# Optimization experiments

Measured on AMD Instinct MI355X. Metric: run time of the kernel, lower is better.

Reference implementation:

```python
import jax, jax.numpy as jnp
import numpy as np

B, IN, OUT = 512, 4096, 11008


def setup_inputs() -> dict:
    key = jax.random.key(0)
    k_x, k_stored, k_sign, k_scale, k_bias = jax.random.split(key, 5)
    x = jax.random.normal(k_x, (B, IN), dtype=jnp.float32)
    # QINS encoding: stored uint8 magnitude in [1, 255], sign in {-1, +1}
    stored = jax.random.randint(k_stored, (OUT, IN), 1, 256, dtype=jnp.int32)
    sign = 2 * jax.random.randint(k_sign, (OUT, IN), 0, 2, dtype=jnp.int32) - 1
    # log-range from from_linear's fallback calibration: weights in [e^-10, e^0]
    log_min = jnp.asarray(-10.0, dtype=jnp.float32)
    log_max = jnp.asarray(0.0, dtype=jnp.float32)
    # per-channel calibration scale, clamped to [0.5, 2.0] in from_linear
    scale = jax.random.uniform(k_scale, (OUT,), dtype=jnp.float32, minval=0.5, maxval=2.0)
    bias = jax.random.normal(k_bias, (OUT,), dtype=jnp.float32) * 0.01
    return {"x": x, "stored": stored, "sign": sign, "log_min": log_min,
            "log_max": log_max, "scale": scale, "bias": bias}


def reference(x, stored, sign, log_min, log_max, scale, bias):
    # Reconstruct fp32 weight from log-scale uint8 encoding (QINS)
    normalized = (255.0 - stored.astype(jnp.float32)) / 254.0      # [OUT, IN]
    log_w = log_min + normalized * (log_max - log_min)
    weight = sign.astype(jnp.float32) * jnp.exp(log_w)             # [OUT, IN]
    # y = (x @ W^T + b) * scale   (per-output-channel scale)
    out = jnp.einsum('bi,oi->bo', x, weight) + bias
    return out * scale
```

## Files before the change

kernel.cpp:

```cpp
#include <hip/hip_runtime.h>
#include <hip/hip_bf16.h>

#define B_DIM   512
#define IN_DIM  4096
#define OUT_DIM 11008

typedef __bf16 bf16x4 __attribute__((ext_vector_type(4)));
typedef __bf16 bf16x8 __attribute__((ext_vector_type(8)));
typedef float  floatx4 __attribute__((ext_vector_type(4)));

__global__ __launch_bounds__(256) void conv_x_kernel(
    const float* __restrict__ x, __bf16* __restrict__ xb) {
  int idx = blockIdx.x * blockDim.x + threadIdx.x;
  float4 v = ((const float4*)x)[idx];
  bf16x4 o;
  o[0] = (__bf16)v.x; o[1] = (__bf16)v.y; o[2] = (__bf16)v.z; o[3] = (__bf16)v.w;
  ((bf16x4*)xb)[idx] = o;
}

__device__ __forceinline__ void gl_lds16(const __bf16* g, __bf16* l) {
  __builtin_amdgcn_global_load_lds(
      (const __attribute__((address_space(1))) void*)g,
      (__attribute__((address_space(3))) void*)l, 16, 0, 0);
}

__device__ __forceinline__ void memfence_barrier() {
  asm volatile("" ::: "memory");
  __builtin_amdgcn_s_barrier();
  asm volatile("" ::: "memory");
}

__device__ __forceinline__ __bf16 dec1(int s, int g, float lmin, float slope) {
  return (__bf16)(__expf(lmin + (float)(255 - s) * slope) * (float)g);
}

__global__ __launch_bounds__(256, 2) void fused_qins_gemm_kernel(
    const __bf16* __restrict__ A,
    const int* __restrict__ stored,
    const int* __restrict__ sign,
    const float* __restrict__ logmin, const float* __restrict__ logmax,
    const float* __restrict__ scale, const float* __restrict__ bias,
    float* __restrict__ out) {
  constexpr int K = IN_DIM, N = OUT_DIM;
  constexpr int BK = 32;

  __shared__ __align__(16) __bf16 sA[2 * 128 * BK];
  __shared__ __align__(16) __bf16 sB[128 * BK];

  const int tid  = threadIdx.x;
  const int lane = tid & 63;
  const int wave = tid >> 6;
  const int wm   = (wave >> 1) * 64;
  const int wn   = (wave & 1) * 64;
  const int m16  = lane & 15;
  const int q    = lane >> 4;

  const int wg  = blockIdx.x;
  const int g   = (wg & 7) * 43 + (wg >> 3);
  const int bn0 = (g >> 2) * 128;
  const int bm0 = (g & 3) * 128;

  const float lmin  = logmin[0];
  const float slope = (logmax[0] - lmin) * (1.0f / 254.0f);

  const int r0 = tid >> 2;
  const int c0 = (tid & 3) * 8;
  const __bf16* gA0 = A + (bm0 + r0) * K + c0;
  const __bf16* gA1 = A + (bm0 + r0 + 64) * K + c0;

  const int rB = tid >> 1;
  const int kh = (tid & 1) * 16;
  const int* pS = stored + (size_t)(bn0 + rB) * K + kh;
  const int* pG = sign   + (size_t)(bn0 + rB) * K + kh;
  __bf16* lB = sB + rB * BK + kh;

  floatx4 acc[4][4] = {};

  gl_lds16(gA0, sA + tid * 8);
  gl_lds16(gA1, sA + 2048 + tid * 8);
  int4 s0 = ((const int4*)pS)[0], s1 = ((const int4*)pS)[1],
       s2 = ((const int4*)pS)[2], s3 = ((const int4*)pS)[3];
  int4 g0 = ((const int4*)pG)[0], g1 = ((const int4*)pG)[1],
       g2 = ((const int4*)pG)[2], g3 = ((const int4*)pG)[3];

  for (int kt = 0; kt < K; kt += BK) {
    const int cur = (kt >> 5) & 1;
    __bf16* sAc = sA + cur * 4096;
    __bf16* sAn = sA + (cur ^ 1) * 4096;

    bf16x8 w0, w1;
    w0[0] = dec1(s0.x, g0.x, lmin, slope);
    w0[1] = dec1(s0.y, g0.y, lmin, slope);
    w0[2] = dec1(s0.z, g0.z, lmin, slope);
    w0[3] = dec1(s0.w, g0.w, lmin, slope);
    w0[4] = dec1(s1.x, g1.x, lmin, slope);
    w0[5] = dec1(s1.y, g1.y, lmin, slope);
    w0[6] = dec1(s1.z, g1.z, lmin, slope);
    w0[7] = dec1(s1.w, g1.w, lmin, slope);
    w1[0] = dec1(s2.x, g2.x, lmin, slope);
    w1[1] = dec1(s2.y, g2.y, lmin, slope);
    w1[2] = dec1(s2.z, g2.z, lmin, slope);
    w1[3] = dec1(s2.w, g2.w, lmin, slope);
    w1[4] = dec1(s3.x, g3.x, lmin, slope);
    w1[5] = dec1(s3.y, g3.y, lmin, slope);
    w1[6] = dec1(s3.z, g3.z, lmin, slope);
    w1[7] = dec1(s3.w, g3.w, lmin, slope);

    memfence_barrier();

    *(bf16x8*)lB       = w0;
    *(bf16x8*)(lB + 8) = w1;

    asm volatile("s_waitcnt vmcnt(0) lgkmcnt(0)" ::: "memory");

    if (kt + BK < K) {
      gl_lds16(gA0 + kt + BK, sAn + tid * 8);
      gl_lds16(gA1 + kt + BK, sAn + 2048 + tid * 8);
      const int4* nS = (const int4*)(pS + kt + BK);
      const int4* nG = (const int4*)(pG + kt + BK);
      s0 = nS[0]; s1 = nS[1]; s2 = nS[2]; s3 = nS[3];
      g0 = nG[0]; g1 = nG[1]; g2 = nG[2]; g3 = nG[3];
    }

    memfence_barrier();

    bf16x8 afr[4], bfr[4];
#pragma unroll
    for (int i = 0; i < 4; ++i)
      afr[i] = *(const bf16x8*)&sAc[(wm + i * 16 + m16) * BK + q * 8];
#pragma unroll
    for (int i = 0; i < 4; ++i)
      bfr[i] = *(const bf16x8*)&sB[(wn + i * 16 + m16) * BK + q * 8];

#pragma unroll
    for (int mi = 0; mi < 4; ++mi)
#pragma unroll
      for (int ni = 0; ni < 4; ++ni)
        acc[mi][ni] = __builtin_amdgcn_mfma_f32_16x16x32_bf16(
            afr[mi], bfr[ni], acc[mi][ni], 0, 0, 0);
  }

#pragma unroll
  for (int ni = 0; ni < 4; ++ni) {
    const int col = bn0 + wn + ni * 16 + m16;
    const float sc = scale[col];
    const float bb = bias[col] * sc;
#pragma unroll
    for (int mi = 0; mi < 4; ++mi) {
#pragma unroll
      for (int r = 0; r < 4; ++r) {
        const int row = bm0 + wm + mi * 16 + q * 4 + r;
        out[row * N + col] = acc[mi][ni][r] * sc + bb;
      }
    }
  }
}

extern "C" void kernel_launch(void* const* d_in, const int* in_sizes, int n_in,
                              void* d_out, int out_size, void* d_ws, size_t ws_size,
                              hipStream_t stream) {
  const float* x      = (const float*)d_in[0];
  const int*   stored = (const int*)d_in[1];
  const int*   sign   = (const int*)d_in[2];
  const float* logmin = (const float*)d_in[3];
  const float* logmax = (const float*)d_in[4];
  const float* scale  = (const float*)d_in[5];
  const float* bias   = (const float*)d_in[6];
  float* out = (float*)d_out;

  __bf16* wsX = (__bf16*)d_ws;

  conv_x_kernel<<<2048, 256, 0, stream>>>(x, wsX);
  fused_qins_gemm_kernel<<<344, 256, 0, stream>>>(
      wsX, stored, sign, logmin, logmax, scale, bias, out);
}
```

Before: 516.8 us.

## Halve N tile, prefetch weights two stages ahead, and swizzle/pad LDS

The output tile shrinks from 128x128 to 128x64, doubling the grid to 688 workgroups so more CUs stay busy, and each thread decodes 8 weights per step instead of 16. The stored/sign int loads are now issued two K-steps ahead through a manually unrolled double-register pipeline, with a partial vmcnt wait instead of a full drain. The A tile uses an XOR swizzle and the B tile a padded row stride to reduce LDS bank conflicts. In exchange, each block reuses A over fewer columns, so total A traffic roughly doubles, and the final prefetches wrap around to redundant loads at k=0.

```diff
diff --git a/kernel.cpp b/kernel.cpp
--- a/kernel.cpp
+++ b/kernel.cpp
@@ -34,6 +34,20 @@
   return (__bf16)(__expf(lmin + (float)(255 - s) * slope) * (float)g);
 }
 
+__device__ __forceinline__ bf16x8 dec8(int4 sl, int4 sh, int4 gl, int4 gh,
+                                       float lmin, float slope) {
+  bf16x8 w;
+  w[0] = dec1(sl.x, gl.x, lmin, slope);
+  w[1] = dec1(sl.y, gl.y, lmin, slope);
+  w[2] = dec1(sl.z, gl.z, lmin, slope);
+  w[3] = dec1(sl.w, gl.w, lmin, slope);
+  w[4] = dec1(sh.x, gh.x, lmin, slope);
+  w[5] = dec1(sh.y, gh.y, lmin, slope);
+  w[6] = dec1(sh.z, gh.z, lmin, slope);
+  w[7] = dec1(sh.w, gh.w, lmin, slope);
+  return w;
+}
+
 __global__ __launch_bounds__(256, 2) void fused_qins_gemm_kernel(
     const __bf16* __restrict__ A,
     const int* __restrict__ stored,
@@ -43,105 +57,86 @@
     float* __restrict__ out) {
   constexpr int K = IN_DIM, N = OUT_DIM;
   constexpr int BK = 32;
+  constexpr int NIT = K / BK;
+  constexpr int SBS = 40;
 
-  __shared__ __align__(16) __bf16 sA[2 * 128 * BK];
-  __shared__ __align__(16) __bf16 sB[128 * BK];
+  __shared__ __align__(16) __bf16 sA[2][128 * BK];
+  __shared__ __align__(16) __bf16 sB[64 * SBS];
 
   const int tid  = threadIdx.x;
   const int lane = tid & 63;
   const int wave = tid >> 6;
   const int wm   = (wave >> 1) * 64;
-  const int wn   = (wave & 1) * 64;
+  const int wn   = (wave & 1) * 32;
   const int m16  = lane & 15;
   const int q    = lane >> 4;
 
   const int wg  = blockIdx.x;
-  const int g   = (wg & 7) * 43 + (wg >> 3);
-  const int bn0 = (g >> 2) * 128;
+  const int g   = (wg & 7) * 86 + (wg >> 3);
   const int bm0 = (g & 3) * 128;
+  const int bn0 = (g >> 2) * 64;
 
   const float lmin  = logmin[0];
   const float slope = (logmax[0] - lmin) * (1.0f / 254.0f);
 
-  const int r0 = tid >> 2;
-  const int c0 = (tid & 3) * 8;
-  const __bf16* gA0 = A + (bm0 + r0) * K + c0;
-  const __bf16* gA1 = A + (bm0 + r0 + 64) * K + c0;
+  const int rA   = tid >> 2;
+  const int slot = (tid & 3) ^ (rA & 3);
+  const __bf16* gA0 = A + (bm0 + rA) * K + slot * 8;
+  const __bf16* gA1 = A + (bm0 + rA + 64) * K + slot * 8;
+  const int aReadSlot = q ^ (m16 & 3);
 
-  const int rB = tid >> 1;
-  const int kh = (tid & 1) * 16;
-  const int* pS = stored + (size_t)(bn0 + rB) * K + kh;
-  const int* pG = sign   + (size_t)(bn0 + rB) * K + kh;
-  __bf16* lB = sB + rB * BK + kh;
+  const int rB = tid >> 2;
+  const int kq = (tid & 3) * 8;
+  const int* pS = stored + (size_t)(bn0 + rB) * K + kq;
+  const int* pG = sign   + (size_t)(bn0 + rB) * K + kq;
+  __bf16* lB = sB + rB * SBS + kq;
 
-  floatx4 acc[4][4] = {};
+  floatx4 acc[4][2] = {};
 
-  gl_lds16(gA0, sA + tid * 8);
-  gl_lds16(gA1, sA + 2048 + tid * 8);
-  int4 s0 = ((const int4*)pS)[0], s1 = ((const int4*)pS)[1],
-       s2 = ((const int4*)pS)[2], s3 = ((const int4*)pS)[3];
-  int4 g0 = ((const int4*)pG)[0], g1 = ((const int4*)pG)[1],
-       g2 = ((const int4*)pG)[2], g3 = ((const int4*)pG)[3];
+  int4 s0a = ((const int4*)pS)[0], s1a = ((const int4*)pS)[1];
+  int4 g0a = ((const int4*)pG)[0], g1a = ((const int4*)pG)[1];
+  int4 s0b = ((const int4*)(pS + BK))[0], s1b = ((const int4*)(pS + BK))[1];
+  int4 g0b = ((const int4*)(pG + BK))[0], g1b = ((const int4*)(pG + BK))[1];
+  gl_lds16(gA0, sA[0] + tid * 8);
+  gl_lds16(gA1, sA[0] + 2048 + tid * 8);
 
-  for (int kt = 0; kt < K; kt += BK) {
-    const int cur = (kt >> 5) & 1;
-    __bf16* sAc = sA + cur * 4096;
-    __bf16* sAn = sA + (cur ^ 1) * 4096;
+#define BODY(i, S0, S1, G0, G1, CUR, NXT)                                     \
+  {                                                                           \
+    bf16x8 w = dec8(S0, S1, G0, G1, lmin, slope);                             \
+    const int kt2 = ((i) + 2 < NIT) ? ((i) + 2) * BK : 0;                     \
+    S0 = ((const int4*)(pS + kt2))[0]; S1 = ((const int4*)(pS + kt2))[1];     \
+    G0 = ((const int4*)(pG + kt2))[0]; G1 = ((const int4*)(pG + kt2))[1];     \
+    memfence_barrier();                   \
+    *(bf16x8*)lB = w;                                                         \
+    asm volatile("s_waitcnt vmcnt(4) lgkmcnt(0)" ::: "memory");               \
+    const int kt1 = ((i) + 1 < NIT) ? ((i) + 1) * BK : 0;                     \
+    gl_lds16(gA0 + kt1, (NXT) + tid * 8);                                     \
+    gl_lds16(gA1 + kt1, (NXT) + 2048 + tid * 8);                              \
+    memfence_barrier();                    \
+    bf16x8 afr[4], bfr[2];                                                    \
+    _Pragma("unroll")                                                         \
+    for (int ii = 0; ii < 4; ++ii)                                            \
+      afr[ii] = *(const bf16x8*)&(CUR)[(wm + ii * 16 + m16) * BK +            \
+                                       aReadSlot * 8];                        \
+    _Pragma("unroll")                                                         \
+    for (int ii = 0; ii < 2; ++ii)                                            \
+      bfr[ii] = *(const bf16x8*)&sB[(wn + ii * 16 + m16) * SBS + q * 8];      \
+    _Pragma("unroll")                                                         \
+    for (int mi = 0; mi < 4; ++mi)                                            \
+      _Pragma("unroll")                                                       \
+      for (int ni = 0; ni < 2; ++ni)                                          \
+        acc[mi][ni] = __builtin_amdgcn_mfma_f32_16x16x32_bf16(                \
+            afr[mi], bfr[ni], acc[mi][ni], 0, 0, 0);                          \
+  }
 
-    bf16x8 w0, w1;
-    w0[0] = dec1(s0.x, g0.x, lmin, slope);
-    w0[1] = dec1(s0.y, g0.y, lmin, slope);
-    w0[2] = dec1(s0.z, g0.z, lmin, slope);
-    w0[3] = dec1(s0.w, g0.w, lmin, slope);
-    w0[4] = dec1(s1.x, g1.x, lmin, slope);
-    w0[5] = dec1(s1.y, g1.y, lmin, slope);
-    w0[6] = dec1(s1.z, g1.z, lmin, slope);
-    w0[7] = dec1(s1.w, g1.w, lmin, slope);
-    w1[0] = dec1(s2.x, g2.x, lmin, slope);
-    w1[1] = dec1(s2.y, g2.y, lmin, slope);
-    w1[2] = dec1(s2.z, g2.z, lmin, slope);
-    w1[3] = dec1(s2.w, g2.w, lmin, slope);
-    w1[4] = dec1(s3.x, g3.x, lmin, slope);
-    w1[5] = dec1(s3.y, g3.y, lmin, slope);
-    w1[6] = dec1(s3.z, g3.z, lmin, slope);
-    w1[7] = dec1(s3.w, g3.w, lmin, slope);
-
-    memfence_barrier();
-
-    *(bf16x8*)lB       = w0;
-    *(bf16x8*)(lB + 8) = w1;
-
-    asm volatile("s_waitcnt vmcnt(0) lgkmcnt(0)" ::: "memory");
-
-    if (kt + BK < K) {
-      gl_lds16(gA0 + kt + BK, sAn + tid * 8);
-      gl_lds16(gA1 + kt + BK, sAn + 2048 + tid * 8);
-      const int4* nS = (const int4*)(pS + kt + BK);
-      const int4* nG = (const int4*)(pG + kt + BK);
-      s0 = nS[0]; s1 = nS[1]; s2 = nS[2]; s3 = nS[3];
-      g0 = nG[0]; g1 = nG[1]; g2 = nG[2]; g3 = nG[3];
-    }
-
-    memfence_barrier();
-
-    bf16x8 afr[4], bfr[4];
-#pragma unroll
-    for (int i = 0; i < 4; ++i)
-      afr[i] = *(const bf16x8*)&sAc[(wm + i * 16 + m16) * BK + q * 8];
-#pragma unroll
-    for (int i = 0; i < 4; ++i)
-      bfr[i] = *(const bf16x8*)&sB[(wn + i * 16 + m16) * BK + q * 8];
+  for (int it = 0; it < NIT; it += 2) {
+    BODY(it,     s0a, s1a, g0a, g1a, sA[0], sA[1]);
+    BODY(it + 1, s0b, s1b, g0b, g1b, sA[1], sA[0]);
+  }
+#undef BODY
 
 #pragma unroll
-    for (int mi = 0; mi < 4; ++mi)
-#pragma unroll
-      for (int ni = 0; ni < 4; ++ni)
-        acc[mi][ni] = __builtin_amdgcn_mfma_f32_16x16x32_bf16(
-            afr[mi], bfr[ni], acc[mi][ni], 0, 0, 0);
-  }
-
-#pragma unroll
-  for (int ni = 0; ni < 4; ++ni) {
+  for (int ni = 0; ni < 2; ++ni) {
     const int col = bn0 + wn + ni * 16 + m16;
     const float sc = scale[col];
     const float bb = bias[col] * sc;
@@ -171,6 +166,6 @@
   __bf16* wsX = (__bf16*)d_ws;
 
   conv_x_kernel<<<2048, 256, 0, stream>>>(x, wsX);
-  fused_qins_gemm_kernel<<<344, 256, 0, stream>>>(
+  fused_qins_gemm_kernel<<<688, 256, 0, stream>>>(
       wsX, stored, sign, logmin, logmax, scale, bias, out);
 }
```

New measurement: 461.9 us. -10.6%, faster.
